# Performance work log

Hardware: AMD Instinct MI355X
Metric: run time of the kernel (lower is better)

The kernel has to match this reference:

```python
import jax, jax.numpy as jnp
import numpy as np

N_NODES = 100000
N_EDGES = 1600000
IN_CH = 128
HID = 256
OUT_CH = 128
N_GRAPHS = 2048


def setup_inputs() -> dict:
    key = jax.random.key(0)
    ks = jax.random.split(key, 12)
    x = jax.random.normal(ks[0], (N_NODES, IN_CH), dtype=jnp.float32)
    edge_index = jax.random.randint(ks[1], (2, N_EDGES), 0, N_NODES, dtype=jnp.int32)
    batch = jnp.sort(jax.random.randint(ks[2], (N_NODES,), 0, N_GRAPHS, dtype=jnp.int32))
    s = lambda k, shp, fan: jax.random.normal(k, shp, dtype=jnp.float32) / np.sqrt(fan)
    params = {
        # SAGEConv1: lin_l (applied to aggregated neighbors, has bias) and lin_r (root)
        "W1l": s(ks[3], (IN_CH, HID), IN_CH), "b1": jnp.zeros((HID,), jnp.float32),
        "W1r": s(ks[4], (IN_CH, HID), IN_CH),
        # SAGEConv2
        "W2l": s(ks[5], (HID, HID), HID), "b2": jnp.zeros((HID,), jnp.float32),
        "W2r": s(ks[6], (HID, HID), HID),
        # MLP head
        "W3": s(ks[7], (HID, HID), HID), "b3": jnp.zeros((HID,), jnp.float32),
        "W4": s(ks[8], (HID, OUT_CH), HID), "b4": jnp.zeros((OUT_CH,), jnp.float32),
    }
    return {"x": x, "edge_index": edge_index, "batch": batch, **params}


def _sage_conv(x, src, dst, Wl, bl, Wr, num_nodes):
    # PyG SAGEConv (aggr='mean'): out_i = Wl @ mean_{j->i} x_j + bl + Wr @ x_i
    agg = jax.ops.segment_sum(x[src], dst, num_segments=num_nodes)  # [N, C]
    cnt = jax.ops.segment_sum(jnp.ones((src.shape[0],), x.dtype), dst, num_segments=num_nodes)
    mean = agg / jnp.maximum(cnt, 1.0)[:, None]
    return mean @ Wl + bl + x @ Wr


def reference(x, edge_index, batch, W1l, b1, W1r, W2l, b2, W2r, W3, b3, W4, b4):
    src, dst = edge_index[0], edge_index[1]
    h = jax.nn.relu(_sage_conv(x, src, dst, W1l, b1, W1r, N_NODES))
    # dropout is identity in eval mode
    h = jax.nn.relu(_sage_conv(h, src, dst, W2l, b2, W2r, N_NODES))
    # global_mean_pool over graphs
    psum = jax.ops.segment_sum(h, batch, num_segments=N_GRAPHS)  # [G, HID]
    gcnt = jax.ops.segment_sum(jnp.ones((h.shape[0],), h.dtype), batch, num_segments=N_GRAPHS)
    pooled = psum / jnp.maximum(gcnt, 1.0)[:, None]
    # MLP head
    hidden = jax.nn.relu(pooled @ W3 + b3)
    return hidden @ W4 + b4  # [G, OUT_CH]
```

## Files before the change

### kernel.cpp

```cpp
#include <hip/hip_runtime.h>

#define N_NODES 100000
#define N_EDGES 1600000
#define IN_CH 128
#define HID 256
#define OUT_CH 128
#define N_GRAPHS 2048

#define NBUK 391
#define CHUNK 8192

typedef __attribute__((ext_vector_type(8))) short bf16x8;
typedef __attribute__((ext_vector_type(4))) float f32x4;
typedef __attribute__((ext_vector_type(2))) float f32x2;

__device__ inline unsigned short f2b(float f) {
    unsigned int u = __builtin_bit_cast(unsigned int, f);
    u = (u + 0x7FFF + ((u >> 16) & 1)) >> 16;
    return (unsigned short)u;
}
__device__ inline float b2f(unsigned short h) {
    unsigned int u = (unsigned int)h << 16;
    return __builtin_bit_cast(float, u);
}

#define GLOAD_LDS16(gsrc, ldst)                                                   \
    __builtin_amdgcn_global_load_lds(                                             \
        (const __attribute__((address_space(1))) void*)(gsrc),                    \
        (__attribute__((address_space(3))) void*)(ldst), 16, 0, 0)

#define SCAN_ITEMS 8
#define SCAN_TILE (256 * SCAN_ITEMS)

__global__ void scan1_k(const int* __restrict__ in, int* __restrict__ out,
                        int n, int* __restrict__ total) {
    __shared__ int wsum[4];
    int base = blockIdx.x * SCAN_TILE + (int)threadIdx.x * SCAN_ITEMS;
    int v[SCAN_ITEMS];
    int s = 0;
    #pragma unroll
    for (int i = 0; i < SCAN_ITEMS; ++i) {
        v[i] = (base + i < n) ? in[base + i] : 0;
        s += v[i];
    }
    int lane = threadIdx.x & 63, wid = threadIdx.x >> 6;
    int incl = s;
    #pragma unroll
    for (int off = 1; off < 64; off <<= 1) {
        int t = __shfl_up(incl, off, 64);
        if (lane >= off) incl += t;
    }
    if (lane == 63) wsum[wid] = incl;
    __syncthreads();
    int wprefix = 0;
    #pragma unroll
    for (int w = 0; w < 4; ++w)
        if (w < wid) wprefix += wsum[w];
    int run = wprefix + incl - s;
    #pragma unroll
    for (int i = 0; i < SCAN_ITEMS; ++i) {
        if (base + i < n) out[base + i] = run;
        run += v[i];
    }
    if (threadIdx.x == 255) *total = wprefix + incl;
}

__global__ void bucket_count_k(const int* __restrict__ dst, int* __restrict__ bcnt, int E) {
    __shared__ int cnt[NBUK];
    int tid = threadIdx.x;
    for (int i = tid; i < NBUK; i += 256) cnt[i] = 0;
    __syncthreads();
    int e0 = blockIdx.x * CHUNK;
    int eend = min(e0 + CHUNK, E);
    for (int e = e0 + tid; e < eend; e += 256)
        atomicAdd(&cnt[dst[e] >> 8], 1);
    __syncthreads();
    for (int i = tid; i < NBUK; i += 256)
        if (cnt[i]) atomicAdd(&bcnt[i], cnt[i]);
}

__global__ void bin_scatter_k(const int* __restrict__ src, const int* __restrict__ dst,
                              const int* __restrict__ bbase, int* __restrict__ bcur,
                              uint2* __restrict__ staging, int E) {
    __shared__ int cnt[NBUK];
    __shared__ int gbase[NBUK];
    int tid = threadIdx.x;
    for (int i = tid; i < NBUK; i += 256) cnt[i] = 0;
    __syncthreads();
    int e0 = blockIdx.x * CHUNK;
    int eend = min(e0 + CHUNK, E);
    for (int e = e0 + tid; e < eend; e += 256)
        atomicAdd(&cnt[dst[e] >> 8], 1);
    __syncthreads();
    for (int i = tid; i < NBUK; i += 256) {
        int c = cnt[i];
        gbase[i] = c ? (bbase[i] + atomicAdd(&bcur[i], c)) : 0;
        cnt[i] = 0;
    }
    __syncthreads();
    for (int e = e0 + tid; e < eend; e += 256) {
        int d = dst[e];
        int b = d >> 8;
        int l = atomicAdd(&cnt[b], 1);
        uint2 p; p.x = (unsigned)src[e]; p.y = (unsigned)d;
        staging[(size_t)gbase[b] + l] = p;
    }
}

__global__ void csr_build_k(const uint2* __restrict__ staging, const int* __restrict__ bbase,
                            int* __restrict__ row_ofs, int* __restrict__ csr) {
    __shared__ int ldeg[256];
    __shared__ int lofs[256];
    __shared__ int wsum[4];
    int b = blockIdx.x, tid = threadIdx.x;
    int base = bbase[b];
    int cnt = bbase[b + 1] - base;
    ldeg[tid] = 0;
    __syncthreads();
    const uint2* sp = staging + base;
    for (int i = tid; i < cnt; i += 256)
        atomicAdd(&ldeg[sp[i].y & 255], 1);
    __syncthreads();
    int v = ldeg[tid];
    int lane = tid & 63, wid = tid >> 6;
    int incl = v;
    #pragma unroll
    for (int off = 1; off < 64; off <<= 1) {
        int t = __shfl_up(incl, off, 64);
        if (lane >= off) incl += t;
    }
    if (lane == 63) wsum[wid] = incl;
    __syncthreads();
    int wprefix = 0;
    #pragma unroll
    for (int w = 0; w < 4; ++w)
        if (w < wid) wprefix += wsum[w];
    int excl = wprefix + incl - v;
    lofs[tid] = excl;
    int node = b * 256 + tid;
    if (node < N_NODES) row_ofs[node] = base + excl;
    if (b == NBUK - 1 && tid == 0) row_ofs[N_NODES] = N_EDGES;
    ldeg[tid] = 0;
    __syncthreads();
    for (int i = tid; i < cnt; i += 256) {
        uint2 p = sp[i];
        int d = (int)p.y & 255;
        int pos = atomicAdd(&ldeg[d], 1);
        csr[base + lofs[d] + pos] = (int)p.x;
    }
}

__global__ void wt_concat_k(const float* __restrict__ Wl, const float* __restrict__ Wr,
                            unsigned short* __restrict__ out, int K1, int K2, int N) {
    int idx = blockIdx.x * blockDim.x + threadIdx.x;
    int KT = K1 + K2;
    if (idx >= N * KT) return;
    int n = idx / KT, k = idx % KT;
    float v = (k < K1) ? Wl[(size_t)k * N + n] : Wr[(size_t)(k - K1) * N + n];
    out[idx] = f2b(v);
}

__global__ void f2b8_k(const float* __restrict__ in, unsigned short* __restrict__ outb,
                       unsigned char* __restrict__ out8, size_t n8) {
    size_t i = (size_t)blockIdx.x * blockDim.x + threadIdx.x;
    if (i >= n8) return;
    float4 a = ((const float4*)in)[i * 2];
    float4 b = ((const float4*)in)[i * 2 + 1];
    unsigned short ob[8];
    ob[0] = f2b(a.x); ob[1] = f2b(a.y); ob[2] = f2b(a.z); ob[3] = f2b(a.w);
    ob[4] = f2b(b.x); ob[5] = f2b(b.y); ob[6] = f2b(b.z); ob[7] = f2b(b.w);
    ((uint4*)outb)[i] = *(const uint4*)ob;
    int w0 = 0, w1 = 0;
    w0 = __builtin_amdgcn_cvt_pk_fp8_f32(a.x, a.y, w0, false);
    w0 = __builtin_amdgcn_cvt_pk_fp8_f32(a.z, a.w, w0, true);
    w1 = __builtin_amdgcn_cvt_pk_fp8_f32(b.x, b.y, w1, false);
    w1 = __builtin_amdgcn_cvt_pk_fp8_f32(b.z, b.w, w1, true);
    uint2 o8; o8.x = (unsigned int)w0; o8.y = (unsigned int)w1;
    ((uint2*)out8)[i] = o8;
}

template <int C>
__global__ void agg_f8_k(const unsigned char* __restrict__ X8, const int* __restrict__ row_ofs,
                         const int* __restrict__ csr, unsigned short* __restrict__ out, int n) {
    constexpr int GL = C / 16;
    constexpr int NG = 64 / GL;
    int w = (int)((blockIdx.x * blockDim.x + threadIdx.x) >> 6);
    int lane = threadIdx.x & 63;
    if (w >= n) return;
    int g = lane / GL, il = lane % GL;
    int s = row_ofs[w], e = row_ofs[w + 1];
    float a[16];
    #pragma unroll
    for (int t = 0; t < 16; ++t) a[t] = 0.f;

    int j = s + g;
    for (; j + NG < e; j += 2 * NG) {
        int i0 = csr[j], i1 = csr[j + NG];
        uint4 r0 = *(const uint4*)&X8[(size_t)i0 * C + il * 16];
        uint4 r1 = *(const uint4*)&X8[(size_t)i1 * C + il * 16];
        const unsigned int* q0 = (const unsigned int*)&r0;
        const unsigned int* q1 = (const unsigned int*)&r1;
        #pragma unroll
        for (int t = 0; t < 4; ++t) {
            f32x2 lo = __builtin_amdgcn_cvt_pk_f32_fp8(q0[t], false);
            f32x2 hi = __builtin_amdgcn_cvt_pk_f32_fp8(q0[t], true);
            a[t * 4 + 0] += lo.x; a[t * 4 + 1] += lo.y;
            a[t * 4 + 2] += hi.x; a[t * 4 + 3] += hi.y;
        }
        #pragma unroll
        for (int t = 0; t < 4; ++t) {
            f32x2 lo = __builtin_amdgcn_cvt_pk_f32_fp8(q1[t], false);
            f32x2 hi = __builtin_amdgcn_cvt_pk_f32_fp8(q1[t], true);
            a[t * 4 + 0] += lo.x; a[t * 4 + 1] += lo.y;
            a[t * 4 + 2] += hi.x; a[t * 4 + 3] += hi.y;
        }
    }
    if (j < e) {
        int i0 = csr[j];
        uint4 r0 = *(const uint4*)&X8[(size_t)i0 * C + il * 16];
        const unsigned int* q0 = (const unsigned int*)&r0;
        #pragma unroll
        for (int t = 0; t < 4; ++t) {
            f32x2 lo = __builtin_amdgcn_cvt_pk_f32_fp8(q0[t], false);
            f32x2 hi = __builtin_amdgcn_cvt_pk_f32_fp8(q0[t], true);
            a[t * 4 + 0] += lo.x; a[t * 4 + 1] += lo.y;
            a[t * 4 + 2] += hi.x; a[t * 4 + 3] += hi.y;
        }
    }

    #pragma unroll
    for (int m = GL; m < 64; m <<= 1)
        #pragma unroll
        for (int t = 0; t < 16; ++t) a[t] += __shfl_xor(a[t], m, 64);

    if (g == 0) {
        float inv = 1.0f / (float)max(e - s, 1);
        uint4 o0, o1;
        unsigned short* p0 = (unsigned short*)&o0;
        unsigned short* p1 = (unsigned short*)&o1;
        #pragma unroll
        for (int t = 0; t < 8; ++t) p0[t] = f2b(a[t] * inv);
        #pragma unroll
        for (int t = 0; t < 8; ++t) p1[t] = f2b(a[8 + t] * inv);
        *(uint4*)&out[(size_t)w * C + il * 16] = o0;
        *(uint4*)&out[(size_t)w * C + il * 16 + 8] = o1;
    }
}

__global__ void pool_mean_k(const unsigned short* __restrict__ H, const int* __restrict__ batch,
                            float* __restrict__ pooled, int G, int n) {
    int g = (int)((blockIdx.x * blockDim.x + threadIdx.x) >> 6);
    int lane = threadIdx.x & 63;
    if (g >= G) return;
    int lo = 0, hi = n;
    while (lo < hi) { int mid = (lo + hi) >> 1; if (batch[mid] < g) lo = mid + 1; else hi = mid; }
    int s = lo;
    hi = n;
    while (lo < hi) { int mid = (lo + hi) >> 1; if (batch[mid] < g + 1) lo = mid + 1; else hi = mid; }
    int e = lo;

    float a0 = 0.f, a1 = 0.f, a2 = 0.f, a3 = 0.f;
    float b0 = 0.f, b1 = 0.f, b2 = 0.f, b3 = 0.f;
    int r = s;
    for (; r + 4 <= e; r += 4) {
        ushort4 t0 = ((const ushort4*)(H + (size_t)(r + 0) * HID))[lane];
        ushort4 t1 = ((const ushort4*)(H + (size_t)(r + 1) * HID))[lane];
        ushort4 t2 = ((const ushort4*)(H + (size_t)(r + 2) * HID))[lane];
        ushort4 t3 = ((const ushort4*)(H + (size_t)(r + 3) * HID))[lane];
        a0 += b2f(t0.x); a1 += b2f(t0.y); a2 += b2f(t0.z); a3 += b2f(t0.w);
        b0 += b2f(t1.x); b1 += b2f(t1.y); b2 += b2f(t1.z); b3 += b2f(t1.w);
        a0 += b2f(t2.x); a1 += b2f(t2.y); a2 += b2f(t2.z); a3 += b2f(t2.w);
        b0 += b2f(t3.x); b1 += b2f(t3.y); b2 += b2f(t3.z); b3 += b2f(t3.w);
    }
    for (; r < e; ++r) {
        ushort4 t = ((const ushort4*)(H + (size_t)r * HID))[lane];
        a0 += b2f(t.x); a1 += b2f(t.y); a2 += b2f(t.z); a3 += b2f(t.w);
    }
    float inv = 1.0f / (float)max(e - s, 1);
    float4 o; o.x = (a0 + b0) * inv; o.y = (a1 + b1) * inv;
    o.z = (a2 + b2) * inv; o.w = (a3 + b3) * inv;
    ((float4*)(pooled + (size_t)g * HID))[lane] = o;
}

__launch_bounds__(256)
__global__ void mfma_gemm_k(const unsigned short* __restrict__ A1, int K1,
                            const unsigned short* __restrict__ A2, int K2,
                            const unsigned short* __restrict__ Bt,
                            const float* __restrict__ bias, int M, int Nfull,
                            void* __restrict__ Cptr, unsigned char* __restrict__ f8out,
                            int c_bf16, int do_relu) {
    __shared__ short ldsA[3 * 4096];
    __shared__ short ldsB[3 * 4096];
    int tid = threadIdx.x, lane = tid & 63;
    int wid = tid >> 6, wm = wid >> 1, wn = wid & 1;
    int row0 = blockIdx.x * 128, col0 = blockIdx.y * 128;
    int q = lane >> 4, l15 = lane & 15;
    int KT = K1 + K2;
    int nk = KT / 32;

    int rr = tid >> 2;
    int c8 = ((tid & 3) ^ (rr & 3)) * 8;
    int dof = wid * 512;

    auto stage = [&](int t, short* bA, short* bB) {
        int kt = t * 32;
        const unsigned short* Asrc; int kk, Ks;
        if (kt < K1) { Asrc = A1; kk = kt; Ks = K1; }
        else         { Asrc = A2; kk = kt - K1; Ks = K2; }
        #pragma unroll
        for (int h = 0; h < 2; ++h) {
            int r = h * 64 + rr;
            int gr = min(row0 + r, M - 1);
            GLOAD_LDS16(Asrc + (size_t)gr * Ks + kk + c8, bA + h * 2048 + dof);
            GLOAD_LDS16(Bt + (size_t)(col0 + r) * KT + kt + c8, bB + h * 2048 + dof);
        }
    };

    f32x4 acc[4][4] = {};

    stage(0, ldsA, ldsB);
    stage(1, ldsA + 4096, ldsB + 4096);
    stage(2, ldsA + 8192, ldsB + 8192);

    int bi = 0;
    for (int t = 0; t < nk; ++t) {
        if (t + 2 < nk)      asm volatile("s_waitcnt vmcnt(8)" ::: "memory");
        else if (t + 1 < nk) asm volatile("s_waitcnt vmcnt(4)" ::: "memory");
        else                 asm volatile("s_waitcnt vmcnt(0)" ::: "memory");
        asm volatile("s_barrier" ::: "memory");

        short* bA = ldsA + bi * 4096;
        short* bB = ldsB + bi * 4096;
        bf16x8 af[4], bfr[4];
        #pragma unroll
        for (int i = 0; i < 4; ++i) {
            int r = wm * 64 + i * 16 + l15;
            af[i] = *(const bf16x8*)&bA[r * 32 + (q ^ (r & 3)) * 8];
        }
        #pragma unroll
        for (int j = 0; j < 4; ++j) {
            int r = wn * 64 + j * 16 + l15;
            bfr[j] = *(const bf16x8*)&bB[r * 32 + (q ^ (r & 3)) * 8];
        }
        #pragma unroll
        for (int i = 0; i < 4; ++i)
            #pragma unroll
            for (int j = 0; j < 4; ++j)
                acc[i][j] = __builtin_amdgcn_mfma_f32_16x16x32_bf16(af[i], bfr[j], acc[i][j], 0, 0, 0);

        asm volatile("s_barrier" ::: "memory");
        if (t + 3 < nk) stage(t + 3, bA, bB);
        bi = (bi == 2) ? 0 : bi + 1;
    }

    #pragma unroll
    for (int i = 0; i < 4; ++i) {
        #pragma unroll
        for (int reg = 0; reg < 4; ++reg) {
            int r = row0 + wm * 64 + i * 16 + q * 4 + reg;
            if (r < M) {
                #pragma unroll
                for (int j = 0; j < 4; ++j) {
                    int cc = col0 + wn * 64 + j * 16 + l15;
                    float v = acc[i][j][reg] + bias[cc];
                    if (do_relu) v = fmaxf(v, 0.f);
                    if (c_bf16) ((unsigned short*)Cptr)[(size_t)r * Nfull + cc] = f2b(v);
                    else        ((float*)Cptr)[(size_t)r * Nfull + cc] = v;
                    if (f8out) {
                        int w8 = __builtin_amdgcn_cvt_pk_fp8_f32(v, v, 0, false);
                        f8out[(size_t)r * Nfull + cc] = (unsigned char)(w8 & 0xFF);
                    }
                }
            }
        }
    }
}

#define BM_ 64
#define BK_ 16

template <int BN_>
__launch_bounds__(256)
__global__ void gemm2_k(const float* __restrict__ A1, const float* __restrict__ B1, int K1,
                        const float* __restrict__ bias, float* __restrict__ C,
                        int M, int N, int do_relu) {
    constexpr int TCOLS = BN_ / 8;
    constexpr int TROWS = 256 / TCOLS;
    constexpr int TM = BM_ / TROWS;
    __shared__ float As[BK_][BM_ + 4];
    __shared__ float Bs[BK_][BN_ + 4];
    int tid = threadIdx.x;
    int row0 = blockIdx.x * BM_;
    int col0 = blockIdx.y * BN_;
    int tx = tid % TCOLS, ty = tid / TCOLS;

    float acc[TM][8];
    #pragma unroll
    for (int i = 0; i < TM; ++i)
        #pragma unroll
        for (int j = 0; j < 8; ++j) acc[i][j] = 0.f;

    int ar = tid >> 2;
    int ak = (tid & 3) * 4;

    for (int kt = 0; kt < K1; kt += BK_) {
        {
            int r = row0 + ar;
            int rc = min(r, M - 1);
            float4 v = *(const float4*)(A1 + (size_t)rc * K1 + kt + ak);
            As[ak + 0][ar] = v.x;
            As[ak + 1][ar] = v.y;
            As[ak + 2][ar] = v.z;
            As[ak + 3][ar] = v.w;
        }
        {
            #pragma unroll
            for (int h = 0; h < BN_ / 64; ++h) {
                int idx = h * 256 + tid;
                int kr = idx / (BN_ / 4);
                int c4 = idx % (BN_ / 4);
                float4 v = *(const float4*)(B1 + (size_t)(kt + kr) * N + col0 + c4 * 4);
                *(float4*)&Bs[kr][c4 * 4] = v;
            }
        }
        __syncthreads();

        #pragma unroll
        for (int k = 0; k < BK_; ++k) {
            float a[TM], b[8];
            #pragma unroll
            for (int v = 0; v < TM / 4; ++v)
                *(float4*)&a[v * 4] = *(const float4*)&As[k][ty * TM + v * 4];
            *(float4*)&b[0] = *(const float4*)&Bs[k][tx * 8];
            *(float4*)&b[4] = *(const float4*)&Bs[k][tx * 8 + 4];
            #pragma unroll
            for (int i = 0; i < TM; ++i)
                #pragma unroll
                for (int j = 0; j < 8; ++j) acc[i][j] = fmaf(a[i], b[j], acc[i][j]);
        }
        __syncthreads();
    }

    float bv[8];
    #pragma unroll
    for (int j = 0; j < 8; ++j) bv[j] = bias[col0 + tx * 8 + j];
    #pragma unroll
    for (int i = 0; i < TM; ++i) {
        int r = row0 + ty * TM + i;
        if (r < M) {
            float* cp = C + (size_t)r * N + col0 + tx * 8;
            float o[8];
            #pragma unroll
            for (int j = 0; j < 8; ++j) {
                float v = acc[i][j] + bv[j];
                o[j] = do_relu ? fmaxf(v, 0.f) : v;
            }
            *(float4*)(cp + 0) = *(float4*)&o[0];
            *(float4*)(cp + 4) = *(float4*)&o[4];
        }
    }
}

extern "C" void kernel_launch(void* const* d_in, const int* in_sizes, int n_in,
                              void* d_out, int out_size, void* d_ws, size_t ws_size,
                              hipStream_t stream) {
    const float* x    = (const float*)d_in[0];
    const int*   ei   = (const int*)d_in[1];
    const int*   batch= (const int*)d_in[2];
    const float* W1l  = (const float*)d_in[3];
    const float* b1   = (const float*)d_in[4];
    const float* W1r  = (const float*)d_in[5];
    const float* W2l  = (const float*)d_in[6];
    const float* b2   = (const float*)d_in[7];
    const float* W2r  = (const float*)d_in[8];
    const float* W3   = (const float*)d_in[9];
    const float* b3   = (const float*)d_in[10];
    const float* W4   = (const float*)d_in[11];
    const float* b4   = (const float*)d_in[12];
    float* out = (float*)d_out;

    const int N = N_NODES, E = N_EDGES, G = N_GRAPHS;
    const int* src = ei;
    const int* dst = ei + E;

    char* ws = (char*)d_ws;
    size_t off = 0;
    auto alloc = [&](size_t bytes) -> char* {
        off = (off + 255) & ~(size_t)255;
        char* p = ws + off;
        off += bytes;
        return p;
    };
    int* bcnt    = (int*)alloc((size_t)NBUK * 4);
    int* bcur    = (int*)alloc((size_t)NBUK * 4);
    size_t zero_span = (size_t)((char*)(bcur + NBUK) - (char*)bcnt);
    int* bbase   = (int*)alloc((size_t)(NBUK + 1) * 4);
    int* row_ofs = (int*)alloc((size_t)(N + 1) * 4);
    uint2* staging = (uint2*)alloc((size_t)E * 8);
    int* csr     = (int*)alloc((size_t)E * 4);
    unsigned short* xb    = (unsigned short*)alloc((size_t)N * IN_CH * 2);
    unsigned short* mean1 = (unsigned short*)alloc((size_t)N * IN_CH * 2);
    unsigned short* h1    = (unsigned short*)alloc((size_t)N * HID * 2);
    unsigned short* mean2 = (unsigned short*)alloc((size_t)N * HID * 2);
    unsigned short* h2    = xb;
    unsigned char*  x8    = (unsigned char*)alloc((size_t)N * IN_CH);
    unsigned char*  h1f8  = (unsigned char*)alloc((size_t)N * HID);
    unsigned short* W1T   = (unsigned short*)alloc((size_t)HID * (IN_CH + IN_CH) * 2);
    unsigned short* W2T   = (unsigned short*)alloc((size_t)HID * (HID + HID) * 2);
    float* pooled = (float*)alloc((size_t)G * HID * 4);
    float* hidden = (float*)alloc((size_t)G * HID * 4);
    (void)ws_size;

    hipMemsetAsync(bcnt, 0, zero_span, stream);

    const int EB = (E + CHUNK - 1) / CHUNK;
    bucket_count_k<<<EB, 256, 0, stream>>>(dst, bcnt, E);
    scan1_k<<<1, 256, 0, stream>>>(bcnt, bbase, NBUK, bbase + NBUK);
    bin_scatter_k<<<EB, 256, 0, stream>>>(src, dst, bbase, bcur, staging, E);
    csr_build_k<<<NBUK, 256, 0, stream>>>(staging, bbase, row_ofs, csr);

    wt_concat_k<<<(HID * 2 * IN_CH + 255) / 256, 256, 0, stream>>>(W1l, W1r, W1T, IN_CH, IN_CH, HID);
    wt_concat_k<<<(HID * 2 * HID + 255) / 256, 256, 0, stream>>>(W2l, W2r, W2T, HID, HID, HID);
    f2b8_k<<<(int)(((size_t)N * IN_CH / 8 + 255) / 256), 256, 0, stream>>>(
        x, xb, x8, (size_t)N * IN_CH / 8);

    const int MB = (N + 127) / 128;

    agg_f8_k<IN_CH><<<(N + 3) / 4, 256, 0, stream>>>(x8, row_ofs, csr, mean1, N);
    mfma_gemm_k<<<dim3(MB, HID / 128), 256, 0, stream>>>(
        mean1, IN_CH, xb, IN_CH, W1T, b1, N, HID, h1, h1f8, 1, 1);

    agg_f8_k<HID><<<(N + 3) / 4, 256, 0, stream>>>(h1f8, row_ofs, csr, mean2, N);
    mfma_gemm_k<<<dim3(MB, HID / 128), 256, 0, stream>>>(
        mean2, HID, h1, HID, W2T, b2, N, HID, h2, nullptr, 1, 1);

    pool_mean_k<<<(G + 3) / 4, 256, 0, stream>>>(h2, batch, pooled, G, N);

    gemm2_k<HID><<<dim3(G / BM_, 1), 256, 0, stream>>>(
        pooled, W3, HID, b3, hidden, G, HID, 1);
    gemm2_k<OUT_CH><<<dim3(G / BM_, 1), 256, 0, stream>>>(
        hidden, W4, HID, b4, out, G, OUT_CH, 0);
}
```

Before: 534.9 us.

## Pack CSR staging entries, fuse prep kernels, retile MLP head GEMMs

Edge staging entries are packed into one 32-bit word (src shifted left by 8, low byte of dst) instead of a uint2, halving staging traffic in bin_scatter and csr_build. The two weight transpose kernels and the x conversion kernel are merged into one prep kernel to cut launches. The head GEMMs use small 32x32 tiles, giving many more blocks for better parallelism on the 2048-row problem. Packing assumes src is below 2^24, which holds for 100k nodes.

```diff
diff --git a/kernel.cpp b/kernel.cpp
--- a/kernel.cpp
+++ b/kernel.cpp
@@ -81,7 +81,7 @@
 
 __global__ void bin_scatter_k(const int* __restrict__ src, const int* __restrict__ dst,
                               const int* __restrict__ bbase, int* __restrict__ bcur,
-                              uint2* __restrict__ staging, int E) {
+                              unsigned* __restrict__ staging, int E) {
     __shared__ int cnt[NBUK];
     __shared__ int gbase[NBUK];
     int tid = threadIdx.x;
@@ -102,12 +102,11 @@
         int d = dst[e];
         int b = d >> 8;
         int l = atomicAdd(&cnt[b], 1);
-        uint2 p; p.x = (unsigned)src[e]; p.y = (unsigned)d;
-        staging[(size_t)gbase[b] + l] = p;
-    }
-}
-
-__global__ void csr_build_k(const uint2* __restrict__ staging, const int* __restrict__ bbase,
+        staging[(size_t)gbase[b] + l] = ((unsigned)src[e] << 8) | (unsigned)(d & 255);
+    }
+}
+
+__global__ void csr_build_k(const unsigned* __restrict__ staging, const int* __restrict__ bbase,
                             int* __restrict__ row_ofs, int* __restrict__ csr) {
     __shared__ int ldeg[256];
     __shared__ int lofs[256];
@@ -117,9 +116,9 @@
     int cnt = bbase[b + 1] - base;
     ldeg[tid] = 0;
     __syncthreads();
-    const uint2* sp = staging + base;
+    const unsigned* sp = staging + base;
     for (int i = tid; i < cnt; i += 256)
-        atomicAdd(&ldeg[sp[i].y & 255], 1);
+        atomicAdd(&ldeg[sp[i] & 255], 1);
     __syncthreads();
     int v = ldeg[tid];
     int lane = tid & 63, wid = tid >> 6;
@@ -143,40 +142,50 @@
     ldeg[tid] = 0;
     __syncthreads();
     for (int i = tid; i < cnt; i += 256) {
-        uint2 p = sp[i];
-        int d = (int)p.y & 255;
+        unsigned p = sp[i];
+        int d = (int)(p & 255);
         int pos = atomicAdd(&ldeg[d], 1);
-        csr[base + lofs[d] + pos] = (int)p.x;
-    }
-}
-
-__global__ void wt_concat_k(const float* __restrict__ Wl, const float* __restrict__ Wr,
-                            unsigned short* __restrict__ out, int K1, int K2, int N) {
-    int idx = blockIdx.x * blockDim.x + threadIdx.x;
-    int KT = K1 + K2;
-    if (idx >= N * KT) return;
-    int n = idx / KT, k = idx % KT;
-    float v = (k < K1) ? Wl[(size_t)k * N + n] : Wr[(size_t)(k - K1) * N + n];
-    out[idx] = f2b(v);
-}
-
-__global__ void f2b8_k(const float* __restrict__ in, unsigned short* __restrict__ outb,
-                       unsigned char* __restrict__ out8, size_t n8) {
-    size_t i = (size_t)blockIdx.x * blockDim.x + threadIdx.x;
-    if (i >= n8) return;
-    float4 a = ((const float4*)in)[i * 2];
-    float4 b = ((const float4*)in)[i * 2 + 1];
-    unsigned short ob[8];
-    ob[0] = f2b(a.x); ob[1] = f2b(a.y); ob[2] = f2b(a.z); ob[3] = f2b(a.w);
-    ob[4] = f2b(b.x); ob[5] = f2b(b.y); ob[6] = f2b(b.z); ob[7] = f2b(b.w);
-    ((uint4*)outb)[i] = *(const uint4*)ob;
-    int w0 = 0, w1 = 0;
-    w0 = __builtin_amdgcn_cvt_pk_fp8_f32(a.x, a.y, w0, false);
-    w0 = __builtin_amdgcn_cvt_pk_fp8_f32(a.z, a.w, w0, true);
-    w1 = __builtin_amdgcn_cvt_pk_fp8_f32(b.x, b.y, w1, false);
-    w1 = __builtin_amdgcn_cvt_pk_fp8_f32(b.z, b.w, w1, true);
-    uint2 o8; o8.x = (unsigned int)w0; o8.y = (unsigned int)w1;
-    ((uint2*)out8)[i] = o8;
+        csr[base + lofs[d] + pos] = (int)(p >> 8);
+    }
+}
+
+__global__ void prep_k(const float* __restrict__ W1l, const float* __restrict__ W1r,
+                       unsigned short* __restrict__ W1T,
+                       const float* __restrict__ W2l, const float* __restrict__ W2r,
+                       unsigned short* __restrict__ W2T,
+                       const float* __restrict__ x, unsigned short* __restrict__ xb,
+                       unsigned char* __restrict__ x8) {
+    int b = blockIdx.x;
+    if (b < 256) {
+        int idx = b * 256 + (int)threadIdx.x;
+        const int KT = 2 * IN_CH;
+        int n = idx / KT, k = idx % KT;
+        float v = (k < IN_CH) ? W1l[(size_t)k * HID + n] : W1r[(size_t)(k - IN_CH) * HID + n];
+        W1T[idx] = f2b(v);
+    } else if (b < 768) {
+        int idx = (b - 256) * 256 + (int)threadIdx.x;
+        const int KT = 2 * HID;
+        int n = idx / KT, k = idx % KT;
+        float v = (k < HID) ? W2l[(size_t)k * HID + n] : W2r[(size_t)(k - HID) * HID + n];
+        W2T[idx] = f2b(v);
+    } else {
+        size_t i = (size_t)(b - 768) * 256 + threadIdx.x;
+        size_t n8 = (size_t)N_NODES * IN_CH / 8;
+        if (i >= n8) return;
+        float4 a = ((const float4*)x)[i * 2];
+        float4 c = ((const float4*)x)[i * 2 + 1];
+        unsigned short ob[8];
+        ob[0] = f2b(a.x); ob[1] = f2b(a.y); ob[2] = f2b(a.z); ob[3] = f2b(a.w);
+        ob[4] = f2b(c.x); ob[5] = f2b(c.y); ob[6] = f2b(c.z); ob[7] = f2b(c.w);
+        ((uint4*)xb)[i] = *(const uint4*)ob;
+        int w0 = 0, w1 = 0;
+        w0 = __builtin_amdgcn_cvt_pk_fp8_f32(a.x, a.y, w0, false);
+        w0 = __builtin_amdgcn_cvt_pk_fp8_f32(a.z, a.w, w0, true);
+        w1 = __builtin_amdgcn_cvt_pk_fp8_f32(c.x, c.y, w1, false);
+        w1 = __builtin_amdgcn_cvt_pk_fp8_f32(c.z, c.w, w1, true);
+        uint2 o8; o8.x = (unsigned int)w0; o8.y = (unsigned int)w1;
+        ((uint2*)x8)[i] = o8;
+    }
 }
 
 template <int C>
@@ -376,89 +385,48 @@
     }
 }
 
-#define BM_ 64
-#define BK_ 16
-
-template <int BN_>
-__launch_bounds__(256)
-__global__ void gemm2_k(const float* __restrict__ A1, const float* __restrict__ B1, int K1,
-                        const float* __restrict__ bias, float* __restrict__ C,
-                        int M, int N, int do_relu) {
-    constexpr int TCOLS = BN_ / 8;
-    constexpr int TROWS = 256 / TCOLS;
-    constexpr int TM = BM_ / TROWS;
-    __shared__ float As[BK_][BM_ + 4];
-    __shared__ float Bs[BK_][BN_ + 4];
+__global__ void head_gemm_k(const float* __restrict__ A, const float* __restrict__ B,
+                            const float* __restrict__ bias, float* __restrict__ C,
+                            int M, int N, int K, int do_relu) {
+    __shared__ float As[16][33];
+    __shared__ float Bs[16][33];
     int tid = threadIdx.x;
-    int row0 = blockIdx.x * BM_;
-    int col0 = blockIdx.y * BN_;
-    int tx = tid % TCOLS, ty = tid / TCOLS;
-
-    float acc[TM][8];
-    #pragma unroll
-    for (int i = 0; i < TM; ++i)
-        #pragma unroll
-        for (int j = 0; j < 8; ++j) acc[i][j] = 0.f;
-
-    int ar = tid >> 2;
-    int ak = (tid & 3) * 4;
-
-    for (int kt = 0; kt < K1; kt += BK_) {
-        {
-            int r = row0 + ar;
-            int rc = min(r, M - 1);
-            float4 v = *(const float4*)(A1 + (size_t)rc * K1 + kt + ak);
-            As[ak + 0][ar] = v.x;
-            As[ak + 1][ar] = v.y;
-            As[ak + 2][ar] = v.z;
-            As[ak + 3][ar] = v.w;
-        }
-        {
-            #pragma unroll
-            for (int h = 0; h < BN_ / 64; ++h) {
-                int idx = h * 256 + tid;
-                int kr = idx / (BN_ / 4);
-                int c4 = idx % (BN_ / 4);
-                float4 v = *(const float4*)(B1 + (size_t)(kt + kr) * N + col0 + c4 * 4);
-                *(float4*)&Bs[kr][c4 * 4] = v;
-            }
+    int row0 = blockIdx.x * 32, col0 = blockIdx.y * 32;
+    int tx = tid & 15, ty = tid >> 4;
+    float a00 = 0.f, a01 = 0.f, a10 = 0.f, a11 = 0.f;
+
+    for (int kt = 0; kt < K; kt += 16) {
+        if (tid < 128) {
+            int r = tid >> 2, kc = (tid & 3) * 4;
+            float4 v = *(const float4*)(A + (size_t)(row0 + r) * K + kt + kc);
+            As[kc + 0][r] = v.x; As[kc + 1][r] = v.y;
+            As[kc + 2][r] = v.z; As[kc + 3][r] = v.w;
+        } else {
+            int t2 = tid - 128;
+            int kr = t2 >> 3, c4 = (t2 & 7) * 4;
+            float4 v = *(const float4*)(B + (size_t)(kt + kr) * N + col0 + c4);
+            *(float4*)&Bs[kr][c4] = v;
         }
         __syncthreads();
-
-        #pragma unroll
-        for (int k = 0; k < BK_; ++k) {
-            float a[TM], b[8];
-            #pragma unroll
-            for (int v = 0; v < TM / 4; ++v)
-                *(float4*)&a[v * 4] = *(const float4*)&As[k][ty * TM + v * 4];
-            *(float4*)&b[0] = *(const float4*)&Bs[k][tx * 8];
-            *(float4*)&b[4] = *(const float4*)&Bs[k][tx * 8 + 4];
-            #pragma unroll
-            for (int i = 0; i < TM; ++i)
-                #pragma unroll
-                for (int j = 0; j < 8; ++j) acc[i][j] = fmaf(a[i], b[j], acc[i][j]);
+        #pragma unroll
+        for (int k = 0; k < 16; ++k) {
+            float x0 = As[k][ty * 2], x1 = As[k][ty * 2 + 1];
+            float y0 = Bs[k][tx * 2], y1 = Bs[k][tx * 2 + 1];
+            a00 = fmaf(x0, y0, a00); a01 = fmaf(x0, y1, a01);
+            a10 = fmaf(x1, y0, a10); a11 = fmaf(x1, y1, a11);
         }
         __syncthreads();
     }
 
-    float bv[8];
-    #pragma unroll
-    for (int j = 0; j < 8; ++j) bv[j] = bias[col0 + tx * 8 + j];
-    #pragma unroll
-    for (int i = 0; i < TM; ++i) {
-        int r = row0 + ty * TM + i;
-        if (r < M) {
-            float* cp = C + (size_t)r * N + col0 + tx * 8;
-            float o[8];
-            #pragma unroll
-            for (int j = 0; j < 8; ++j) {
-                float v = acc[i][j] + bv[j];
-                o[j] = do_relu ? fmaxf(v, 0.f) : v;
-            }
-            *(float4*)(cp + 0) = *(float4*)&o[0];
-            *(float4*)(cp + 4) = *(float4*)&o[4];
-        }
-    }
+    int r0 = row0 + ty * 2, c0 = col0 + tx * 2;
+    float bv0 = bias[c0], bv1 = bias[c0 + 1];
+    float o00 = a00 + bv0, o01 = a01 + bv1, o10 = a10 + bv0, o11 = a11 + bv1;
+    if (do_relu) {
+        o00 = fmaxf(o00, 0.f); o01 = fmaxf(o01, 0.f);
+        o10 = fmaxf(o10, 0.f); o11 = fmaxf(o11, 0.f);
+    }
+    C[(size_t)r0 * N + c0] = o00;       C[(size_t)r0 * N + c0 + 1] = o01;
+    C[(size_t)(r0 + 1) * N + c0] = o10; C[(size_t)(r0 + 1) * N + c0 + 1] = o11;
 }
 
 extern "C" void kernel_launch(void* const* d_in, const int* in_sizes, int n_in,
@@ -496,7 +464,7 @@
     size_t zero_span = (size_t)((char*)(bcur + NBUK) - (char*)bcnt);
     int* bbase   = (int*)alloc((size_t)(NBUK + 1) * 4);
     int* row_ofs = (int*)alloc((size_t)(N + 1) * 4);
-    uint2* staging = (uint2*)alloc((size_t)E * 8);
+    unsigned* staging = (unsigned*)alloc((size_t)E * 4);
     int* csr     = (int*)alloc((size_t)E * 4);
     unsigned short* xb    = (unsigned short*)alloc((size_t)N * IN_CH * 2);
     unsigned short* mean1 = (unsigned short*)alloc((size_t)N * IN_CH * 2);
@@ -519,10 +487,8 @@
     bin_scatter_k<<<EB, 256, 0, stream>>>(src, dst, bbase, bcur, staging, E);
     csr_build_k<<<NBUK, 256, 0, stream>>>(staging, bbase, row_ofs, csr);
 
-    wt_concat_k<<<(HID * 2 * IN_CH + 255) / 256, 256, 0, stream>>>(W1l, W1r, W1T, IN_CH, IN_CH, HID);
-    wt_concat_k<<<(HID * 2 * HID + 255) / 256, 256, 0, stream>>>(W2l, W2r, W2T, HID, HID, HID);
-    f2b8_k<<<(int)(((size_t)N * IN_CH / 8 + 255) / 256), 256, 0, stream>>>(
-        x, xb, x8, (size_t)N * IN_CH / 8);
+    const int PREP_B = 768 + (int)(((size_t)N * IN_CH / 8 + 255) / 256);
+    prep_k<<<PREP_B, 256, 0, stream>>>(W1l, W1r, W1T, W2l, W2r, W2T, x, xb, x8);
 
     const int MB = (N + 127) / 128;
 
@@ -536,8 +502,8 @@
 
     pool_mean_k<<<(G + 3) / 4, 256, 0, stream>>>(h2, batch, pooled, G, N);
 
-    gemm2_k<HID><<<dim3(G / BM_, 1), 256, 0, stream>>>(
-        pooled, W3, HID, b3, hidden, G, HID, 1);
-    gemm2_k<OUT_CH><<<dim3(G / BM_, 1), 256, 0, stream>>>(
-        hidden, W4, HID, b4, out, G, OUT_CH, 0);
-}
+    head_gemm_k<<<dim3(G / 32, HID / 32), 256, 0, stream>>>(
+        pooled, W3, b3, hidden, G, HID, HID, 1);
+    head_gemm_k<<<dim3(G / 32, OUT_CH / 32), 256, 0, stream>>>(
+        hidden, W4, b4, out, G, OUT_CH, HID, 0);
+}
```

Measured after the change: 495.6 us. -7.4%, faster.
